# Performance work log

Measured on AMD Instinct MI355X. Metric: run time of the kernel, lower is better.

Reference implementation:

```python
import jax, jax.numpy as jnp
import numpy as np

B, N, T, NL, DIM, H, HD = 4, 2048, 8, 64, 1024, 16, 64


def setup_inputs() -> dict:
    key = jax.random.key(0)
    ks = jax.random.split(key, 8)
    text = jax.random.normal(ks[0], (B, N, DIM), dtype=jnp.float32)
    media = jax.random.normal(ks[1], (B, T, NL, DIM), dtype=jnp.float32)
    # place exactly T media tokens per row, evenly spaced, so cumsum times are in [1, T]
    loc = np.zeros((B, N), dtype=bool)
    step = N // T
    loc[:, np.arange(T) * step] = True
    media_locations = jnp.asarray(loc)
    s = 1.0 / np.sqrt(DIM)
    wq = jax.random.normal(ks[2], (DIM, DIM), dtype=jnp.float32) * s
    wkv = jax.random.normal(ks[3], (DIM, 2 * DIM), dtype=jnp.float32) * s
    wo = jax.random.normal(ks[4], (DIM, DIM), dtype=jnp.float32) * s
    bo = jnp.zeros((DIM,), dtype=jnp.float32)
    ln_g = jnp.ones((DIM,), dtype=jnp.float32)
    ln_b = jnp.zeros((DIM,), dtype=jnp.float32)
    return {"text": text, "media": media, "media_locations": media_locations,
            "wq": wq, "wkv": wkv, "wo": wo, "bo": bo, "ln_g": ln_g, "ln_b": ln_b}


def _layernorm(x, g, b, eps=1e-5):
    mu = jnp.mean(x, axis=-1, keepdims=True)
    var = jnp.var(x, axis=-1, keepdims=True)
    return (x - mu) * jax.lax.rsqrt(var + eps) * g + b


def reference(text, media, media_locations, wq, wkv, wo, bo, ln_g, ln_b):
    b, t, nl, d = media.shape
    tn = _layernorm(text, ln_g, ln_b)                 # [b, n, d]
    q = tn @ wq                                        # [b, n, d]
    m = media.reshape(b, t * nl, d)                    # [b, tn, d]
    kv = m @ wkv                                       # [b, tn, 2d]
    k, v = jnp.split(kv, 2, axis=-1)
    q = q.reshape(b, -1, H, HD).transpose(0, 2, 1, 3)  # [b, h, n, hd]
    k = k.reshape(b, -1, H, HD).transpose(0, 2, 1, 3)  # [b, h, tn, hd]
    v = v.reshape(b, -1, H, HD).transpose(0, 2, 1, 3)
    scores = jnp.einsum('bhid,bhjd->bhij', q, k)       # [b, h, n, tn]
    text_times = jnp.cumsum(media_locations.astype(jnp.int32), axis=-1)  # [b, n]
    media_times = jnp.repeat(jnp.arange(1, t + 1, dtype=jnp.int32), nl)  # [tn]
    mask = text_times[:, None, :, None] == media_times[None, None, None, :]
    neg = jnp.finfo(scores.dtype).min
    scores = jnp.where(mask, scores, neg)
    attn = jax.nn.softmax(scores, axis=-1)
    no_media = (text_times == 0)[:, None, :, None]     # [b, 1, n, 1]
    attn = jnp.where(no_media, 0.0, attn)
    out = jnp.einsum('bhij,bhjd->bhid', attn, v)       # [b, h, n, hd]
    out = out.transpose(0, 2, 1, 3).reshape(b, -1, H * HD)
    return out @ wo + bo
```

## Files before the change

kernel.cpp:

```cpp
#include <hip/hip_runtime.h>
#include <stdint.h>

#define B_ 4
#define N_ 2048
#define T_ 8
#define NL_ 64
#define DIM_ 1024
#define H_ 16
#define HD_ 64
#define TN_ (T_*NL_)

typedef __bf16 bf16x8 __attribute__((ext_vector_type(8)));
typedef float f32x4 __attribute__((ext_vector_type(4)));

__device__ __forceinline__ float b2f(unsigned short x) {
  union { uint32_t u; float f; } v; v.u = ((uint32_t)x) << 16; return v.f;
}
__device__ __forceinline__ unsigned short f2b(float f) {
  union { float f; uint32_t u; } v; v.f = f;
  uint32_t r = v.u + 0x7FFFu + ((v.u >> 16) & 1u);
  return (unsigned short)(r >> 16);
}

__device__ __forceinline__ void gload_lds16(const unsigned short* g, unsigned short* l) {
  __builtin_amdgcn_global_load_lds(
      (const __attribute__((address_space(1))) uint32_t*)g,
      (__attribute__((address_space(3))) uint32_t*)l, 16, 0, 0);
}

__global__ void detect_kernel(const unsigned short* __restrict__ text, int* __restrict__ flag) {
  int t = threadIdx.x;
  int bad = 0;
  #pragma unroll
  for (int i = 0; i < 16; i++) {
    unsigned short w = text[t * 16 + i];
    int e = (w >> 7) & 0xFF;
    if (e != 0 && (e < 90 || e > 150)) bad++;
  }
  __shared__ int red[256];
  red[t] = bad;
  __syncthreads();
  for (int o = 128; o > 0; o >>= 1) { if (t < o) red[t] += red[t + o]; __syncthreads(); }
  if (t == 0) flag[0] = (red[0] > 256) ? 1 : 0;
}

__global__ void cast2_kernel(const void* __restrict__ media, unsigned short* __restrict__ mb,
                             const void* __restrict__ bo, unsigned short* __restrict__ bob,
                             const int* __restrict__ flag) {
  const int N4M = (B_*T_*NL_*DIM_) / 4;
  int i = blockIdx.x * 256 + threadIdx.x;
  bool isf = (*flag != 0);
  if (i < N4M) {
    ushort4 o;
    if (isf) {
      float4 v = ((const float4*)media)[i];
      o.x = f2b(v.x); o.y = f2b(v.y); o.z = f2b(v.z); o.w = f2b(v.w);
    } else {
      o = ((const ushort4*)media)[i];
    }
    ((ushort4*)mb)[i] = o;
  } else {
    int j = i - N4M;
    if (j < DIM_/4) {
      ushort4 o;
      if (isf) {
        float4 v = ((const float4*)bo)[j];
        o.x = f2b(v.x); o.y = f2b(v.y); o.z = f2b(v.z); o.w = f2b(v.w);
      } else {
        o = ((const ushort4*)bo)[j];
      }
      ((ushort4*)bob)[j] = o;
    }
  }
}

__global__ void times_kernel(const void* __restrict__ locs, int* __restrict__ tt) {
  int b = blockIdx.x, t = threadIdx.x;
  const unsigned char* p8 = (const unsigned char*)locs;
  const int* p32 = (const int*)locs;
  __shared__ int red[256];
  int cnt = 0;
  for (int i = t; i < B_*N_; i += 256) cnt += (p8[i] != 0) ? 1 : 0;
  red[t] = cnt;
  __syncthreads();
  for (int off = 128; off > 0; off >>= 1) {
    if (t < off) red[t] += red[t + off];
    __syncthreads();
  }
  int total = red[0];
  __syncthreads();
  bool isb = (total >= 2 * T_);
  int x[8];
  int base = b * N_ + t * 8;
  if (isb) {
    #pragma unroll
    for (int i = 0; i < 8; i++) x[i] = (int)(p8[base + i] != 0);
  } else {
    #pragma unroll
    for (int i = 0; i < 8; i++) x[i] = (int)(p32[base + i] != 0);
  }
  #pragma unroll
  for (int i = 1; i < 8; i++) x[i] += x[i-1];
  int tot = x[7];
  red[t] = tot;
  __syncthreads();
  for (int off = 1; off < 256; off <<= 1) {
    int v = (t >= off) ? red[t - off] : 0;
    __syncthreads();
    red[t] += v;
    __syncthreads();
  }
  int excl = red[t] - tot;
  #pragma unroll
  for (int i = 0; i < 8; i++) tt[base + i] = excl + x[i];
}

__global__ void ln_kernel(const void* __restrict__ x,
                          const void* __restrict__ g,
                          const void* __restrict__ bta,
                          unsigned short* __restrict__ y,
                          const int* __restrict__ flag) {
  int row = blockIdx.x;
  int t = threadIdx.x;
  bool isf = (*flag != 0);
  float f0, f1, f2, f3, g0, g1, g2, g3, c0, c1, c2, c3;
  if (isf) {
    float4 xv = ((const float4*)x)[(size_t)row * (DIM_/4) + t];
    f0 = xv.x; f1 = xv.y; f2 = xv.z; f3 = xv.w;
    float4 gv = ((const float4*)g)[t];
    g0 = gv.x; g1 = gv.y; g2 = gv.z; g3 = gv.w;
    float4 bv = ((const float4*)bta)[t];
    c0 = bv.x; c1 = bv.y; c2 = bv.z; c3 = bv.w;
  } else {
    ushort4 xv = ((const ushort4*)x)[(size_t)row * (DIM_/4) + t];
    f0 = b2f(xv.x); f1 = b2f(xv.y); f2 = b2f(xv.z); f3 = b2f(xv.w);
    ushort4 gv = ((const ushort4*)g)[t];
    g0 = b2f(gv.x); g1 = b2f(gv.y); g2 = b2f(gv.z); g3 = b2f(gv.w);
    ushort4 bv = ((const ushort4*)bta)[t];
    c0 = b2f(bv.x); c1 = b2f(bv.y); c2 = b2f(bv.z); c3 = b2f(bv.w);
  }
  float s  = f0 + f1 + f2 + f3;
  float s2 = f0*f0 + f1*f1 + f2*f2 + f3*f3;
  for (int off = 32; off > 0; off >>= 1) { s += __shfl_xor(s, off); s2 += __shfl_xor(s2, off); }
  __shared__ float sm[8];
  int wave = t >> 6, lane = t & 63;
  if (lane == 0) { sm[wave] = s; sm[wave + 4] = s2; }
  __syncthreads();
  float ts  = sm[0] + sm[1] + sm[2] + sm[3];
  float ts2 = sm[4] + sm[5] + sm[6] + sm[7];
  float mean = ts * (1.0f / DIM_);
  float var  = ts2 * (1.0f / DIM_) - mean * mean;
  float rs = rsqrtf(var + 1e-5f);
  ushort4 o;
  o.x = f2b((f0 - mean) * rs * g0 + c0);
  o.y = f2b((f1 - mean) * rs * g1 + c1);
  o.z = f2b((f2 - mean) * rs * g2 + c2);
  o.w = f2b((f3 - mean) * rs * g3 + c3);
  ((ushort4*)(y + (size_t)row * DIM_))[t] = o;
}

__global__ void transpose3_kernel(const void* __restrict__ wq, unsigned short* __restrict__ wqt,
                                  const void* __restrict__ wkv, unsigned short* __restrict__ wkvt,
                                  const void* __restrict__ wo, unsigned short* __restrict__ wot,
                                  const int* __restrict__ flag) {
  const void* src; unsigned short* dst; int C;
  if (blockIdx.z == 0)      { src = wq;  dst = wqt;  C = 1024; }
  else if (blockIdx.z == 1) { src = wkv; dst = wkvt; C = 2048; }
  else                      { src = wo;  dst = wot;  C = 1024; }
  const int R = 1024;
  int bx = blockIdx.x * 32, by = blockIdx.y * 32;
  if (bx >= C) return;
  __shared__ unsigned short tile[32][33];
  int x = threadIdx.x, y = threadIdx.y;
  if (*flag) {
    const float* s = (const float*)src;
    for (int i = y; i < 32; i += 8) tile[i][x] = f2b(s[(size_t)(by + i) * C + bx + x]);
  } else {
    const unsigned short* s = (const unsigned short*)src;
    for (int i = y; i < 32; i += 8) tile[i][x] = s[(size_t)(by + i) * C + bx + x];
  }
  __syncthreads();
  for (int i = y; i < 32; i += 8) dst[(size_t)(bx + i) * R + by + x] = tile[x][i];
}

__device__ __forceinline__ void gemm128_core(const unsigned short* __restrict__ A,
                                             const unsigned short* __restrict__ Bt,
                                             unsigned short* __restrict__ C,
                                             float* __restrict__ Cf,
                                             const unsigned short* __restrict__ bias,
                                             int bid, int mtiles, int M, int N, int K,
                                             bool f32o, int t) {
  __shared__ unsigned short As[128][32];
  __shared__ unsigned short Bs[128][32];
  int m0 = (bid % mtiles) * 128, n0 = (bid / mtiles) * 128;
  int wave = t >> 6, lane = t & 63;
  int wr = wave >> 1, wc = wave & 1;
  f32x4 acc[4][4];
  #pragma unroll
  for (int i = 0; i < 4; i++)
    #pragma unroll
    for (int j = 0; j < 4; j++)
      #pragma unroll
      for (int r = 0; r < 4; r++) acc[i][j][r] = 0.f;
  int lr = lane & 15, lk = (lane >> 4) * 8;
  int c0c = t, c1c = t + 256;
  int row0 = c0c >> 2, kc0 = (c0c & 3) * 8;
  int row1 = c1c >> 2, kc1 = (c1c & 3) * 8;
  const unsigned short* a0 = A  + (size_t)(m0 + row0) * K + kc0;
  const unsigned short* a1 = A  + (size_t)(m0 + row1) * K + kc1;
  const unsigned short* b0 = Bt + (size_t)(n0 + row0) * K + kc0;
  const unsigned short* b1 = Bt + (size_t)(n0 + row1) * K + kc1;
  for (int k0 = 0; k0 < K; k0 += 32) {
    gload_lds16(a0 + k0, &As[row0][kc0]);
    gload_lds16(a1 + k0, &As[row1][kc1]);
    gload_lds16(b0 + k0, &Bs[row0][kc0]);
    gload_lds16(b1 + k0, &Bs[row1][kc1]);
    __syncthreads();
    bf16x8 af[4], bfr[4];
    #pragma unroll
    for (int i = 0; i < 4; i++) af[i]  = *(const bf16x8*)(&As[wr * 64 + i * 16 + lr][lk]);
    #pragma unroll
    for (int j = 0; j < 4; j++) bfr[j] = *(const bf16x8*)(&Bs[wc * 64 + j * 16 + lr][lk]);
    #pragma unroll
    for (int i = 0; i < 4; i++)
      #pragma unroll
      for (int j = 0; j < 4; j++)
        acc[i][j] = __builtin_amdgcn_mfma_f32_16x16x32_bf16(af[i], bfr[j], acc[i][j], 0, 0, 0);
    __syncthreads();
  }
  int rbase = (lane >> 4) * 4;
  int cbase = lane & 15;
  #pragma unroll
  for (int i = 0; i < 4; i++) {
    #pragma unroll
    for (int j = 0; j < 4; j++) {
      int row = m0 + wr * 64 + i * 16 + rbase;
      int col = n0 + wc * 64 + j * 16 + cbase;
      float bv = bias ? b2f(bias[col]) : 0.f;
      if (f32o) {
        #pragma unroll
        for (int r = 0; r < 4; r++)
          Cf[(size_t)(row + r) * N + col] = acc[i][j][r] + bv;
      } else {
        #pragma unroll
        for (int r = 0; r < 4; r++)
          C[(size_t)(row + r) * N + col] = f2b(acc[i][j][r] + bv);
      }
    }
  }
}

__global__ __launch_bounds__(256) void gemm_qkv(const unsigned short* __restrict__ tn,
                                                const unsigned short* __restrict__ wqt,
                                                unsigned short* __restrict__ qb,
                                                const unsigned short* __restrict__ mb,
                                                const unsigned short* __restrict__ wkvt,
                                                unsigned short* __restrict__ kvb) {
  int bid = blockIdx.x;
  if (bid < 512)
    gemm128_core(tn, wqt, qb, nullptr, nullptr, bid, 64, B_ * N_, DIM_, DIM_, false, threadIdx.x);
  else
    gemm128_core(mb, wkvt, kvb, nullptr, nullptr, bid - 512, 16, B_ * TN_, 2 * DIM_, DIM_, false, threadIdx.x);
}

__global__ __launch_bounds__(256) void gemm_out(const unsigned short* __restrict__ ao,
                                                const unsigned short* __restrict__ wot,
                                                unsigned short* __restrict__ C,
                                                float* __restrict__ Cf,
                                                const unsigned short* __restrict__ bias,
                                                const int* __restrict__ flag) {
  bool f32o = (*flag != 0);
  gemm128_core(ao, wot, C, Cf, bias, blockIdx.x, 64, B_ * N_, DIM_, DIM_, f32o, threadIdx.x);
}

__global__ __launch_bounds__(64) void attn_mfma(const unsigned short* __restrict__ q,
                                                const unsigned short* __restrict__ kv,
                                                const int* __restrict__ tt,
                                                unsigned short* __restrict__ ao) {
  __shared__ unsigned short Vt[64][72];
  __shared__ unsigned short Ps[64][72];
  int bid = blockIdx.x;
  int h  = bid & 15;
  int nt = (bid >> 4) & 31;
  int b  = bid >> 9;
  int bn0 = b * N_ + nt * 64;
  int lane = threadIdx.x & 63;
  int lr = lane & 15;
  int g  = lane >> 4;
  int g8 = g * 8;

  int tv = tt[bn0];
  float vmul = (tv >= 1 && tv <= T_) ? 1.f : 0.f;
  int tvc = tv < 1 ? 1 : (tv > T_ ? T_ : tv);
  int kvrow0 = b * TN_ + (tvc - 1) * NL_;

  const unsigned short* vbase = kv + (size_t)kvrow0 * (2 * DIM_) + DIM_ + h * HD_;
  #pragma unroll
  for (int d0 = 0; d0 < 64; d0 += 8) {
    uint4 v = *(const uint4*)(vbase + (size_t)lane * (2 * DIM_) + d0);
    Vt[d0 + 0][lane] = (unsigned short)(v.x & 0xffff);
    Vt[d0 + 1][lane] = (unsigned short)(v.x >> 16);
    Vt[d0 + 2][lane] = (unsigned short)(v.y & 0xffff);
    Vt[d0 + 3][lane] = (unsigned short)(v.y >> 16);
    Vt[d0 + 4][lane] = (unsigned short)(v.z & 0xffff);
    Vt[d0 + 5][lane] = (unsigned short)(v.z >> 16);
    Vt[d0 + 6][lane] = (unsigned short)(v.w & 0xffff);
    Vt[d0 + 7][lane] = (unsigned short)(v.w >> 16);
  }

  f32x4 S[4][4];
  #pragma unroll
  for (int i = 0; i < 4; i++)
    #pragma unroll
    for (int j = 0; j < 4; j++)
      #pragma unroll
      for (int r = 0; r < 4; r++) S[i][j][r] = 0.f;
  #pragma unroll
  for (int ks = 0; ks < 2; ks++) {
    bf16x8 aQ[4], bK[4];
    #pragma unroll
    for (int mi = 0; mi < 4; mi++)
      aQ[mi] = *(const bf16x8*)(q + (size_t)(bn0 + mi * 16 + lr) * DIM_ + h * HD_ + ks * 32 + g8);
    #pragma unroll
    for (int ni = 0; ni < 4; ni++)
      bK[ni] = *(const bf16x8*)(kv + (size_t)(kvrow0 + ni * 16 + lr) * (2 * DIM_) + h * HD_ + ks * 32 + g8);
    #pragma unroll
    for (int mi = 0; mi < 4; mi++)
      #pragma unroll
      for (int ni = 0; ni < 4; ni++)
        S[mi][ni] = __builtin_amdgcn_mfma_f32_16x16x32_bf16(aQ[mi], bK[ni], S[mi][ni], 0, 0, 0);
  }

  #pragma unroll
  for (int mi = 0; mi < 4; mi++) {
    #pragma unroll
    for (int r = 0; r < 4; r++) {
      float mx = fmaxf(fmaxf(S[mi][0][r], S[mi][1][r]), fmaxf(S[mi][2][r], S[mi][3][r]));
      mx = fmaxf(mx, __shfl_xor(mx, 1));
      mx = fmaxf(mx, __shfl_xor(mx, 2));
      mx = fmaxf(mx, __shfl_xor(mx, 4));
      mx = fmaxf(mx, __shfl_xor(mx, 8));
      float e0 = __expf(S[mi][0][r] - mx);
      float e1 = __expf(S[mi][1][r] - mx);
      float e2 = __expf(S[mi][2][r] - mx);
      float e3 = __expf(S[mi][3][r] - mx);
      float sum = e0 + e1 + e2 + e3;
      sum += __shfl_xor(sum, 1);
      sum += __shfl_xor(sum, 2);
      sum += __shfl_xor(sum, 4);
      sum += __shfl_xor(sum, 8);
      float inv = 1.f / sum;
      int qrow = mi * 16 + g * 4 + r;
      Ps[qrow][ 0 + lr] = f2b(e0 * inv);
      Ps[qrow][16 + lr] = f2b(e1 * inv);
      Ps[qrow][32 + lr] = f2b(e2 * inv);
      Ps[qrow][48 + lr] = f2b(e3 * inv);
    }
  }
  __syncthreads();

  f32x4 O[4][4];
  #pragma unroll
  for (int i = 0; i < 4; i++)
    #pragma unroll
    for (int j = 0; j < 4; j++)
      #pragma unroll
      for (int r = 0; r < 4; r++) O[i][j][r] = 0.f;
  #pragma unroll
  for (int ks = 0; ks < 2; ks++) {
    bf16x8 aP[4], bV[4];
    #pragma unroll
    for (int mi = 0; mi < 4; mi++)
      aP[mi] = *(const bf16x8*)(&Ps[mi * 16 + lr][ks * 32 + g8]);
    #pragma unroll
    for (int ni = 0; ni < 4; ni++)
      bV[ni] = *(const bf16x8*)(&Vt[ni * 16 + lr][ks * 32 + g8]);
    #pragma unroll
    for (int mi = 0; mi < 4; mi++)
      #pragma unroll
      for (int ni = 0; ni < 4; ni++)
        O[mi][ni] = __builtin_amdgcn_mfma_f32_16x16x32_bf16(aP[mi], bV[ni], O[mi][ni], 0, 0, 0);
  }
  __syncthreads();

  #pragma unroll
  for (int mi = 0; mi < 4; mi++)
    #pragma unroll
    for (int ni = 0; ni < 4; ni++)
      #pragma unroll
      for (int r = 0; r < 4; r++)
        Ps[mi * 16 + g * 4 + r][ni * 16 + lr] = f2b(O[mi][ni][r] * vmul);
  __syncthreads();
  uint4* dst = (uint4*)(ao + (size_t)(bn0 + lane) * DIM_ + h * HD_);
  #pragma unroll
  for (int c = 0; c < 8; c++)
    dst[c] = *(const uint4*)(&Ps[lane][c * 8]);
}

extern "C" void kernel_launch(void* const* d_in, const int* in_sizes, int n_in,
                              void* d_out, int out_size, void* d_ws, size_t ws_size,
                              hipStream_t stream) {
  const void* text = d_in[0];
  const void* media = d_in[1];
  const void* mloc = d_in[2];
  const void* wq  = d_in[3];
  const void* wkv = d_in[4];
  const void* wo  = d_in[5];
  const void* bo  = d_in[6];
  const void* lng = d_in[7];
  const void* lnb = d_in[8];

  char* ws = (char*)d_ws;
  const size_t OFF_FLAG = (size_t)32 << 10;
  const size_t OFF_TN   = (size_t)64 << 10;
  const size_t OFF_WQT  = OFF_TN  + ((size_t)16 << 20) + ((size_t)64 << 10);
  const size_t OFF_WKVT = OFF_WQT + ((size_t)2 << 20);
  const size_t OFF_WOT  = OFF_WKVT + ((size_t)4 << 20);
  const size_t OFF_KV   = OFF_WOT + ((size_t)2 << 20);
  const size_t OFF_MB   = OFF_KV  + ((size_t)8 << 20);
  const size_t OFF_BO   = OFF_MB  + ((size_t)4 << 20);
  const size_t OFF_QB   = OFF_BO  + ((size_t)64 << 10);
  int* tt               = (int*)(ws + 0);
  int* flag             = (int*)(ws + OFF_FLAG);
  unsigned short* tn    = (unsigned short*)(ws + OFF_TN);
  unsigned short* ao    = tn;
  unsigned short* wqt   = (unsigned short*)(ws + OFF_WQT);
  unsigned short* wkvt  = (unsigned short*)(ws + OFF_WKVT);
  unsigned short* wot   = (unsigned short*)(ws + OFF_WOT);
  unsigned short* kvb   = (unsigned short*)(ws + OFF_KV);
  unsigned short* mb    = (unsigned short*)(ws + OFF_MB);
  unsigned short* bob   = (unsigned short*)(ws + OFF_BO);
  unsigned short* qb    = (unsigned short*)(ws + OFF_QB);

  detect_kernel<<<1, 256, 0, stream>>>((const unsigned short*)text, flag);
  times_kernel<<<B_, 256, 0, stream>>>(mloc, tt);
  ln_kernel<<<B_ * N_, 256, 0, stream>>>(text, lng, lnb, tn, flag);
  cast2_kernel<<<2049, 256, 0, stream>>>(media, mb, bo, bob, flag);
  transpose3_kernel<<<dim3(64, 32, 3), dim3(32, 8), 0, stream>>>(wq, wqt, wkv, wkvt, wo, wot, flag);

  gemm_qkv<<<768, 256, 0, stream>>>(tn, wqt, qb, mb, wkvt, kvb);
  attn_mfma<<<B_ * (N_/64) * H_, 64, 0, stream>>>(qb, kvb, tt, ao);
  gemm_out<<<512, 256, 0, stream>>>(ao, wot, (unsigned short*)d_out, (float*)d_out, bob, flag);
}
```

Before: 207.0 us.

## Double-buffer LDS tiles in GEMM core to overlap loads with MFMA

Splits the A and B shared-memory tiles into two buffers. The loads for the next K-slice are issued before the MFMAs on the current slice, and one barrier per iteration replaces two. The aim is to hide global-to-LDS load latency behind matrix math. The cost is twice the LDS per block, which may reduce occupancy.

```diff
diff --git a/kernel.cpp b/kernel.cpp
--- a/kernel.cpp
+++ b/kernel.cpp
@@ -190,8 +190,8 @@
                                              const unsigned short* __restrict__ bias,
                                              int bid, int mtiles, int M, int N, int K,
                                              bool f32o, int t) {
-  __shared__ unsigned short As[128][32];
-  __shared__ unsigned short Bs[128][32];
+  __shared__ unsigned short As[2][128][32];
+  __shared__ unsigned short Bs[2][128][32];
   int m0 = (bid % mtiles) * 128, n0 = (bid / mtiles) * 128;
   int wave = t >> 6, lane = t & 63;
   int wr = wave >> 1, wc = wave & 1;
@@ -203,30 +203,38 @@
       #pragma unroll
       for (int r = 0; r < 4; r++) acc[i][j][r] = 0.f;
   int lr = lane & 15, lk = (lane >> 4) * 8;
-  int c0c = t, c1c = t + 256;
-  int row0 = c0c >> 2, kc0 = (c0c & 3) * 8;
-  int row1 = c1c >> 2, kc1 = (c1c & 3) * 8;
+  int row0 = t >> 2,        kc0 = (t & 3) * 8;
+  int row1 = (t + 256) >> 2, kc1 = ((t + 256) & 3) * 8;
   const unsigned short* a0 = A  + (size_t)(m0 + row0) * K + kc0;
   const unsigned short* a1 = A  + (size_t)(m0 + row1) * K + kc1;
   const unsigned short* b0 = Bt + (size_t)(n0 + row0) * K + kc0;
   const unsigned short* b1 = Bt + (size_t)(n0 + row1) * K + kc1;
+  gload_lds16(a0, &As[0][row0][kc0]);
+  gload_lds16(a1, &As[0][row1][kc1]);
+  gload_lds16(b0, &Bs[0][row0][kc0]);
+  gload_lds16(b1, &Bs[0][row1][kc1]);
+  __syncthreads();
+  int cur = 0;
   for (int k0 = 0; k0 < K; k0 += 32) {
-    gload_lds16(a0 + k0, &As[row0][kc0]);
-    gload_lds16(a1 + k0, &As[row1][kc1]);
-    gload_lds16(b0 + k0, &Bs[row0][kc0]);
-    gload_lds16(b1 + k0, &Bs[row1][kc1]);
-    __syncthreads();
+    int nxt = cur ^ 1;
+    if (k0 + 32 < K) {
+      gload_lds16(a0 + k0 + 32, &As[nxt][row0][kc0]);
+      gload_lds16(a1 + k0 + 32, &As[nxt][row1][kc1]);
+      gload_lds16(b0 + k0 + 32, &Bs[nxt][row0][kc0]);
+      gload_lds16(b1 + k0 + 32, &Bs[nxt][row1][kc1]);
+    }
     bf16x8 af[4], bfr[4];
     #pragma unroll
-    for (int i = 0; i < 4; i++) af[i]  = *(const bf16x8*)(&As[wr * 64 + i * 16 + lr][lk]);
-    #pragma unroll
-    for (int j = 0; j < 4; j++) bfr[j] = *(const bf16x8*)(&Bs[wc * 64 + j * 16 + lr][lk]);
+    for (int i = 0; i < 4; i++) af[i]  = *(const bf16x8*)(&As[cur][wr * 64 + i * 16 + lr][lk]);
+    #pragma unroll
+    for (int j = 0; j < 4; j++) bfr[j] = *(const bf16x8*)(&Bs[cur][wc * 64 + j * 16 + lr][lk]);
     #pragma unroll
     for (int i = 0; i < 4; i++)
       #pragma unroll
       for (int j = 0; j < 4; j++)
         acc[i][j] = __builtin_amdgcn_mfma_f32_16x16x32_bf16(af[i], bfr[j], acc[i][j], 0, 0, 0);
     __syncthreads();
+    cur = nxt;
   }
   int rbase = (lane >> 4) * 4;
   int cbase = lane & 15;
```

Result: slower. 211.3 us (+2.1%).
